# Optimization experiments

Measured on AMD Instinct MI355X. Metric: run time of the kernel, lower is better.

The kernel has to match this reference:

```python
import jax, jax.numpy as jnp
import numpy as np

C_IN = 256   # c_m
C_H = 32     # outer_product_dim
C_Z = 128
B, S, N = 1, 128, 256  # batch, msa depth, n_res
EPS = 1e-5


def setup_inputs() -> dict:
    key = jax.random.key(0)
    ks = jax.random.split(key, 10)
    msa = jax.random.normal(ks[0], (B, S, N, C_IN), dtype=jnp.float32)
    mask = jax.random.uniform(ks[1], (B, S, N), dtype=jnp.float32)
    ln_w = jnp.ones((C_IN,), jnp.float32)
    ln_b = jnp.zeros((C_IN,), jnp.float32)
    # weights stored [in, out] (torch Linear transposed)
    wl = jax.random.normal(ks[2], (C_IN, C_H), jnp.float32) / np.sqrt(C_IN)
    bl = jnp.zeros((C_H,), jnp.float32)
    wr = jax.random.normal(ks[3], (C_IN, C_H), jnp.float32) / np.sqrt(C_IN)
    br = jnp.zeros((C_H,), jnp.float32)
    wo = jax.random.normal(ks[4], (C_H * C_H, C_Z), jnp.float32) / np.sqrt(C_H * C_H)
    bo = jnp.zeros((C_Z,), jnp.float32)
    return {"msa_representation": msa, "msa_mask": mask, "ln_w": ln_w, "ln_b": ln_b,
            "wl": wl, "bl": bl, "wr": wr, "br": br, "wo": wo, "bo": bo}


def _layer_norm(x, w, b):
    mu = jnp.mean(x, axis=-1, keepdims=True)
    var = jnp.var(x, axis=-1, keepdims=True)
    return (x - mu) * jax.lax.rsqrt(var + EPS) * w + b


def reference(msa_representation, msa_mask, ln_w, ln_b, wl, bl, wr, br, wo, bo):
    x = _layer_norm(msa_representation, ln_w, ln_b)            # [b,s,i,c_in]
    A = x @ wl + bl                                            # [b,s,i,c]
    Bm = x @ wr + br                                           # [b,s,j,d]
    m = msa_mask
    A = A * m[..., None]
    Bm = Bm * m[..., None]
    outer = jnp.einsum('bsic,bsjd->bijcd', A, Bm)              # [b,i,j,c,d]
    norm = jnp.clip(jnp.einsum('bsi,bsj->bij', m, m), 1.0, None)
    mean_val = outer / norm[..., None, None]
    b_, i_, j_ = mean_val.shape[:3]
    mean_val = mean_val.reshape(b_, i_, j_, -1)                # [b,i,j,c*d]
    return mean_val @ wo + bo                                  # [b,i,j,c_z]
```

## Files before the change

kernel.cpp:

```cpp
#include <hip/hip_runtime.h>
#include <hip/hip_bf16.h>
#include <stdint.h>

#define SDEP 128
#define NRES 256
#define CZQ 128

typedef __bf16 v8bf __attribute__((ext_vector_type(8)));
typedef __bf16 v4bf __attribute__((ext_vector_type(4)));
typedef float v16f __attribute__((ext_vector_type(16)));

__device__ __forceinline__ float dpp_wave_sum(float x) {
  float t;
#define STEP(ctrl)                                                         \
  t = __builtin_bit_cast(float, __builtin_amdgcn_update_dpp(               \
          0, __builtin_bit_cast(int, x), ctrl, 0xF, 0xF, true));           \
  x += t;
  STEP(0x111)
  STEP(0x112)
  STEP(0x114)
  STEP(0x118)
  STEP(0x142)
  STEP(0x143)
#undef STEP
  return x;
}
__device__ __forceinline__ float lane63(float x) {
  return __builtin_bit_cast(float,
      __builtin_amdgcn_readlane(__builtin_bit_cast(int, x), 63));
}

__global__ __launch_bounds__(512, 2) void fusedA_kernel(
    const float* __restrict__ msa, const float* __restrict__ lnw,
    const float* __restrict__ lnb, const float* __restrict__ wl,
    const float* __restrict__ wr, const float* __restrict__ mask,
    const float* __restrict__ wo, const float* __restrict__ bl,
    const float* __restrict__ br,
    __bf16* __restrict__ At2, __bf16* __restrict__ Bt2,
    float* __restrict__ rnorm, __bf16* __restrict__ wot4)
{
  __shared__ __bf16 xs[128 * 258];
  __shared__ __bf16 wcs[16384];
  __shared__ __bf16 Ls[8 * 32 * 36];

  const int i = blockIdx.x, t = threadIdx.x;
  const int w = t >> 6, lane = t & 63;
  const int half = lane >> 5, l31 = lane & 31;
  const int sb = w >> 1, nh = w & 1;

  #pragma unroll
  for (int u = 0; u < 32; ++u) {
    int idx = u * 512 + t;
    int j = idx & 7, n = (idx >> 3) & 31, hf = (idx >> 8) & 1;
    int ks = (idx >> 9) & 15, tile = idx >> 13;
    const float* wsrc = tile ? wr : wl;
    wcs[idx] = (__bf16)wsrc[(ks * 16 + hf * 8 + j) * 32 + n];
  }

  const float4 wv4 = ((const float4*)lnw)[lane];
  const float4 bv4 = ((const float4*)lnb)[lane];

  #pragma unroll 8
  for (int r = 0; r < 16; ++r) {
    const int s = sb * 32 + nh * 16 + r;
    float4 x = ((const float4*)(msa + ((size_t)s * 256 + i) * 256))[lane];
    float s1 = dpp_wave_sum(x.x + x.y + x.z + x.w);
    float s2 = dpp_wave_sum(x.x * x.x + x.y * x.y + x.z * x.z + x.w * x.w);
    float mu = lane63(s1) * (1.f / 256.f);
    float var = lane63(s2) * (1.f / 256.f) - mu * mu;
    float rs = rsqrtf(var + 1e-5f);
    v4bf o;
    o[0] = (__bf16)((x.x - mu) * rs * wv4.x + bv4.x);
    o[1] = (__bf16)((x.y - mu) * rs * wv4.y + bv4.y);
    o[2] = (__bf16)((x.z - mu) * rs * wv4.z + bv4.z);
    o[3] = (__bf16)((x.w - mu) * rs * wv4.w + bv4.w);
    *(v4bf*)(xs + s * 258 + lane * 4) = o;
  }
  __syncthreads();

  v16f acc;
  #pragma unroll
  for (int r = 0; r < 16; ++r) acc[r] = 0.f;

  const __bf16* xrow = xs + (sb * 32 + l31) * 258 + half * 8;
  const __bf16* bbase = wcs + nh * 8192 + half * 256 + l31 * 8;
  #pragma unroll
  for (int ks = 0; ks < 16; ++ks) {
    v8bf a = *(const v8bf*)(xrow + ks * 16);
    v8bf b = *(const v8bf*)(bbase + ks * 512);
    acc = __builtin_amdgcn_mfma_f32_32x32x16_bf16(a, b, acc, 0, 0, 0);
  }

  __bf16* Lw = Ls + w * 32 * 36;
  const float bias = (nh ? br : bl)[l31];
  #pragma unroll
  for (int r = 0; r < 16; ++r) {
    int sl = (r & 3) + 8 * (r >> 2) + 4 * half;
    float mv = mask[(sb * 32 + sl) * NRES + i];
    Lw[l31 * 36 + sl] = (__bf16)((acc[r] + bias) * mv);
  }

  __bf16* dst = nh ? Bt2 : At2;
  const int c = lane >> 1, jq = (lane & 1) * 4;
  #pragma unroll
  for (int o = 0; o < 4; ++o) {
    v4bf v = *(const v4bf*)(Lw + c * 36 + o * 8 + jq);
    *(v4bf*)(dst + ((size_t)i * 16 + sb * 4 + o) * 256 + lane * 4) = v;
  }

  if (i < 128) {
    const int b = i * 2 + (t >> 8), col = t & 255;
    float a0 = 0.f;
    #pragma unroll 4
    for (int s = 0; s < SDEP; ++s)
      a0 += mask[s * NRES + b] * mask[s * NRES + col];
    rnorm[b * NRES + col] = 1.f / fmaxf(a0, 1.f);
  } else {
    #pragma unroll
    for (int u = 0; u < 2; ++u) {
      int idx = (i - 128) * 1024 + u * 512 + t;
      int j = idx & 7, lc = (idx >> 3) & 63, kk = (idx >> 9) & 63, zg = idx >> 15;
      int k = kk * 16 + (lc >> 5) * 8 + j;
      int z = zg * 32 + (lc & 31);
      wot4[idx] = (__bf16)wo[k * CZQ + z];
    }
  }
}

__global__ __launch_bounds__(512, 4) void outer_kernel(
    const __bf16* __restrict__ At2, const __bf16* __restrict__ Bt2,
    const float* __restrict__ rnorm, const __bf16* __restrict__ wot4,
    const float* __restrict__ bo, float* __restrict__ out)
{
  __shared__ char smem[66048];
  __bf16* Ps = (__bf16*)smem;
  float* red = (float*)smem;

  const int tid = threadIdx.x;
  const int w = tid >> 6, lane = tid & 63;
  const int half = lane >> 5, l31 = lane & 31;
  const int bx = blockIdx.x;
  const int by = blockIdx.y;
  const int mt = w >> 1;
  const int nh = w & 1;

  const __bf16* Ap = At2 + ((size_t)(by * 4 + mt)) * 4096 + l31 * 8;
  const __bf16* Bp = Bt2 + ((size_t)(bx * 8 + nh * 4)) * 4096 + l31 * 8;

  v8bf a[8];
  #pragma unroll
  for (int ks = 0; ks < 8; ++ks)
    a[ks] = *(const v8bf*)(Ap + (ks * 2 + half) * 256);

  v16f acc[4];
  #pragma unroll
  for (int t = 0; t < 4; ++t)
    #pragma unroll
    for (int r = 0; r < 16; ++r) acc[t][r] = 0.f;

  #pragma unroll
  for (int t = 0; t < 4; ++t) {
    v8bf b[8];
    #pragma unroll
    for (int ks = 0; ks < 8; ++ks)
      b[ks] = *(const v8bf*)(Bp + t * 4096 + (ks * 2 + half) * 256);
    #pragma unroll
    for (int ks = 0; ks < 8; ++ks)
      acc[t] = __builtin_amdgcn_mfma_f32_32x32x16_bf16(a[ks], b[ks], acc[t], 0, 0, 0);
  }

  #pragma unroll
  for (int t = 0; t < 4; ++t) {
    int jl = nh * 4 + t;
    int p = mt * 8 + jl;
    float rn = rnorm[(by * 4 + mt) * NRES + bx * 8 + jl];
    #pragma unroll
    for (int r = 0; r < 16; ++r) {
      int cc = (r & 3) + 8 * (r >> 2) + 4 * half;
      Ps[p * 1032 + cc * 32 + l31] = (__bf16)(acc[t][r] * rn);
    }
  }

  const int zg = w & 3, kh = w >> 2;
  const __bf16* wp = wot4 + ((size_t)((zg * 64 + kh * 32) * 64) + half * 32 + l31) * 8;
  v8bf wb[8];
  #pragma unroll
  for (int u = 0; u < 8; ++u)
    wb[u] = *(const v8bf*)(wp + u * 512);

  __syncthreads();

  const __bf16* pp = Ps + l31 * 1032 + kh * 512 + half * 8;

  v16f c2;
  #pragma unroll
  for (int r = 0; r < 16; ++r) c2[r] = 0.f;

  #pragma unroll
  for (int g = 0; g < 4; ++g) {
    #pragma unroll
    for (int u = 0; u < 8; ++u) {
      const int kk = g * 8 + u;
      v8bf bb = wb[u];
      if (g < 3) wb[u] = *(const v8bf*)(wp + (kk + 8) * 512);
      v8bf aa = *(const v8bf*)(pp + kk * 16);
      c2 = __builtin_amdgcn_mfma_f32_32x32x16_bf16(aa, bb, c2, 0, 0, 0);
    }
  }
  __syncthreads();

  if (kh == 1) {
    #pragma unroll
    for (int r = 0; r < 16; ++r) {
      int cc = (r & 3) + 8 * (r >> 2) + 4 * half;
      red[zg * 1024 + cc * 32 + l31] = c2[r];
    }
  }
  __syncthreads();

  if (kh == 0) {
    const float bz = bo[zg * 32 + l31];
    #pragma unroll
    for (int r = 0; r < 16; ++r) {
      int cc = (r & 3) + 8 * (r >> 2) + 4 * half;
      float v = c2[r] + red[zg * 1024 + cc * 32 + l31] + bz;
      int i = by * 4 + (cc >> 3), j = bx * 8 + (cc & 7);
      out[((size_t)i * NRES + j) * CZQ + zg * 32 + l31] = v;
    }
  }
}

extern "C" void kernel_launch(void* const* d_in, const int* in_sizes, int n_in,
                              void* d_out, int out_size, void* d_ws, size_t ws_size,
                              hipStream_t stream) {
  const float* msa  = (const float*)d_in[0];
  const float* mask = (const float*)d_in[1];
  const float* lnw  = (const float*)d_in[2];
  const float* lnb  = (const float*)d_in[3];
  const float* wl   = (const float*)d_in[4];
  const float* bl   = (const float*)d_in[5];
  const float* wr   = (const float*)d_in[6];
  const float* br   = (const float*)d_in[7];
  const float* wo   = (const float*)d_in[8];
  const float* bo   = (const float*)d_in[9];
  float* out = (float*)d_out;

  char* ws = (char*)d_ws;
  __bf16* At2   = (__bf16*)(ws);
  __bf16* Bt2   = (__bf16*)(ws + 2097152);
  float*  rnorm = (float*)(ws + 4194304);
  __bf16* wot4  = (__bf16*)(ws + 4456448);

  fusedA_kernel<<<256, 512, 0, stream>>>(msa, lnw, lnb, wl, wr, mask, wo,
                                         bl, br, At2, Bt2, rnorm, wot4);
  outer_kernel<<<dim3(32, 64), 512, 0, stream>>>(At2, Bt2, rnorm, wot4, bo, out);
}
```

Baseline: 153.4 us.

## Use 2x2 MFMA tile per wave in outer product and drop a barrier

Each wave in the outer-product stage now computes a 2x2 grid of 32x32 tiles instead of 1x4, loading A and B fragments per k-step. This cuts global fragment loads per wave and interleaves four independent MFMAs per step. The split-K reduction buffer moves to a separate bf16 LDS region, which removes one __syncthreads but lowers the precision of the partial sum and raises LDS use per block, which may reduce occupancy.

```diff
diff --git a/kernel.cpp b/kernel.cpp
--- a/kernel.cpp
+++ b/kernel.cpp
@@ -132,52 +132,54 @@
     const float* __restrict__ rnorm, const __bf16* __restrict__ wot4,
     const float* __restrict__ bo, float* __restrict__ out)
 {
-  __shared__ char smem[66048];
-  __bf16* Ps = (__bf16*)smem;
-  float* red = (float*)smem;
+  __shared__ char smem[74240];
+  __bf16* Ps   = (__bf16*)smem;
+  __bf16* redb = (__bf16*)(smem + 66048);
 
   const int tid = threadIdx.x;
   const int w = tid >> 6, lane = tid & 63;
   const int half = lane >> 5, l31 = lane & 31;
   const int bx = blockIdx.x;
   const int by = blockIdx.y;
-  const int mt = w >> 1;
-  const int nh = w & 1;
-
-  const __bf16* Ap = At2 + ((size_t)(by * 4 + mt)) * 4096 + l31 * 8;
-  const __bf16* Bp = Bt2 + ((size_t)(bx * 8 + nh * 4)) * 4096 + l31 * 8;
-
-  v8bf a[8];
-  #pragma unroll
-  for (int ks = 0; ks < 8; ++ks)
-    a[ks] = *(const v8bf*)(Ap + (ks * 2 + half) * 256);
-
-  v16f acc[4];
-  #pragma unroll
-  for (int t = 0; t < 4; ++t)
-    #pragma unroll
-    for (int r = 0; r < 16; ++r) acc[t][r] = 0.f;
-
-  #pragma unroll
-  for (int t = 0; t < 4; ++t) {
-    v8bf b[8];
-    #pragma unroll
-    for (int ks = 0; ks < 8; ++ks)
-      b[ks] = *(const v8bf*)(Bp + t * 4096 + (ks * 2 + half) * 256);
-    #pragma unroll
-    for (int ks = 0; ks < 8; ++ks)
-      acc[t] = __builtin_amdgcn_mfma_f32_32x32x16_bf16(a[ks], b[ks], acc[t], 0, 0, 0);
-  }
-
-  #pragma unroll
-  for (int t = 0; t < 4; ++t) {
-    int jl = nh * 4 + t;
-    int p = mt * 8 + jl;
-    float rn = rnorm[(by * 4 + mt) * NRES + bx * 8 + jl];
-    #pragma unroll
-    for (int r = 0; r < 16; ++r) {
-      int cc = (r & 3) + 8 * (r >> 2) + 4 * half;
-      Ps[p * 1032 + cc * 32 + l31] = (__bf16)(acc[t][r] * rn);
+  const int mh = w >> 2;
+  const int nq = w & 3;
+
+  const __bf16* Ap = At2 + ((size_t)(by * 4 + mh * 2)) * 4096 + l31 * 8;
+  const __bf16* Bp = Bt2 + ((size_t)(bx * 8 + nq * 2)) * 4096 + l31 * 8;
+
+  v16f acc[2][2];
+  #pragma unroll
+  for (int a = 0; a < 2; ++a)
+    #pragma unroll
+    for (int b = 0; b < 2; ++b)
+      #pragma unroll
+      for (int r = 0; r < 16; ++r) acc[a][b][r] = 0.f;
+
+  #pragma unroll
+  for (int ks = 0; ks < 8; ++ks) {
+    const int off = (ks * 2 + half) * 256;
+    v8bf a0 = *(const v8bf*)(Ap + off);
+    v8bf a1 = *(const v8bf*)(Ap + 4096 + off);
+    v8bf b0 = *(const v8bf*)(Bp + off);
+    v8bf b1 = *(const v8bf*)(Bp + 4096 + off);
+    acc[0][0] = __builtin_amdgcn_mfma_f32_32x32x16_bf16(a0, b0, acc[0][0], 0, 0, 0);
+    acc[0][1] = __builtin_amdgcn_mfma_f32_32x32x16_bf16(a0, b1, acc[0][1], 0, 0, 0);
+    acc[1][0] = __builtin_amdgcn_mfma_f32_32x32x16_bf16(a1, b0, acc[1][0], 0, 0, 0);
+    acc[1][1] = __builtin_amdgcn_mfma_f32_32x32x16_bf16(a1, b1, acc[1][1], 0, 0, 0);
+  }
+
+  #pragma unroll
+  for (int ti = 0; ti < 2; ++ti) {
+    #pragma unroll
+    for (int tj = 0; tj < 2; ++tj) {
+      const int it = mh * 2 + ti, jt = nq * 2 + tj;
+      const int p = it * 8 + jt;
+      const float rn = rnorm[(by * 4 + it) * NRES + bx * 8 + jt];
+      #pragma unroll
+      for (int r = 0; r < 16; ++r) {
+        int cc = (r & 3) + 8 * (r >> 2) + 4 * half;
+        Ps[p * 1032 + cc * 32 + l31] = (__bf16)(acc[ti][tj][r] * rn);
+      }
     }
   }
 
@@ -207,13 +209,12 @@
       c2 = __builtin_amdgcn_mfma_f32_32x32x16_bf16(aa, bb, c2, 0, 0, 0);
     }
   }
-  __syncthreads();
 
   if (kh == 1) {
     #pragma unroll
     for (int r = 0; r < 16; ++r) {
       int cc = (r & 3) + 8 * (r >> 2) + 4 * half;
-      red[zg * 1024 + cc * 32 + l31] = c2[r];
+      redb[zg * 1024 + cc * 32 + l31] = (__bf16)c2[r];
     }
   }
   __syncthreads();
@@ -223,7 +224,7 @@
     #pragma unroll
     for (int r = 0; r < 16; ++r) {
       int cc = (r & 3) + 8 * (r >> 2) + 4 * half;
-      float v = c2[r] + red[zg * 1024 + cc * 32 + l31] + bz;
+      float v = c2[r] + (float)redb[zg * 1024 + cc * 32 + l31] + bz;
       int i = by * 4 + (cc >> 3), j = bx * 8 + (cc & 7);
       out[((size_t)i * NRES + j) * CZQ + zg * 32 + l31] = v;
     }
```

After: 151.7 us. Within noise of the previous version (-1.1%).
